# Optimization experiments

Hardware: AMD Instinct MI355X
Metric: run time of the kernel (lower is better)

## Reference

```python
import jax, jax.numpy as jnp
import numpy as np

V, E, S, TT, H, C, B = 50000, 300, 128, 12, 512, 3, 128


def setup_inputs() -> dict:
    key = jax.random.key(0)
    ks = jax.random.split(key, 12)
    sc = lambda n: 1.0 / np.sqrt(n)
    return {
        "target_ids": jax.random.randint(ks[0], (B, TT), 0, V),
        "target_len": jax.random.randint(ks[1], (B,), 1, TT + 1, dtype=jnp.int32),
        "left_ids": jax.random.randint(ks[2], (B, S), 0, V),
        "left_len": jax.random.randint(ks[3], (B,), 1, S + 1, dtype=jnp.int32),
        "right_ids": jax.random.randint(ks[4], (B, S), 0, V),
        "right_len": jax.random.randint(ks[5], (B,), 1, S + 1, dtype=jnp.int32),
        "embeddings": jax.random.normal(ks[6], (V, E), jnp.float32) * 0.1,
        "W_left": jax.random.normal(ks[7], (2 * E + H, 4 * H), jnp.float32) * sc(2 * E + H),
        "b_left": jnp.zeros((4 * H,), jnp.float32),
        "W_right": jax.random.normal(ks[8], (2 * E + H, 4 * H), jnp.float32) * sc(2 * E + H),
        "b_right": jnp.zeros((4 * H,), jnp.float32),
        "W_dense": jax.random.normal(ks[9], (2 * H, C), jnp.float32) * sc(2 * H),
        "b_dense": jnp.zeros((C,), jnp.float32),
    }


def _lstm_last_state(x, lens, W, b):
    # x: [B,S,D] inputs, lens: [B]; TF BasicLSTMCell gate order (i, j, f, o), forget_bias=1.0.
    # dynamic_rnn(sequence_length=lens): state frozen once t >= len.
    b_, s_, _ = x.shape
    xs = jnp.swapaxes(x, 0, 1)  # [S,B,D]
    step_mask = jnp.arange(s_)[:, None] < lens[None, :]  # [S,B]
    h0 = jnp.zeros((b_, H), x.dtype)
    c0 = jnp.zeros((b_, H), x.dtype)

    def step(carry, inp):
        h, c = carry
        x_t, m_t = inp
        z = jnp.concatenate([x_t, h], axis=-1) @ W + b  # [B,4H]
        i, j, f, o = jnp.split(z, 4, axis=-1)
        c_new = jax.nn.sigmoid(f + 1.0) * c + jax.nn.sigmoid(i) * jnp.tanh(j)
        h_new = jax.nn.sigmoid(o) * jnp.tanh(c_new)
        m = m_t[:, None]
        return (jnp.where(m, h_new, h), jnp.where(m, c_new, c)), None

    (h, _c), _ = jax.lax.scan(step, (h0, c0), (xs, step_mask))
    return h


def reference(target_ids, target_len, left_ids, left_len, right_ids, right_len,
              embeddings, W_left, b_left, W_right, b_right, W_dense, b_dense):
    # mean target embedding over valid target tokens (variable_len_batch_mean)
    tgt = embeddings[target_ids]  # [B,TT,E]
    tmask = (jnp.arange(TT)[None, :] < target_len[:, None]).astype(tgt.dtype)
    mean_t = jnp.sum(tgt * tmask[:, :, None], axis=1) / target_len[:, None].astype(tgt.dtype)  # [B,E]

    def ctx_inputs(ids):
        e = embeddings[ids]  # [B,S,E]
        # stack([emb, mean_t], axis=2) then reshape -> per-timestep concat [emb_t, mean_t]
        return jnp.concatenate([e, jnp.broadcast_to(mean_t[:, None, :], e.shape)], axis=-1)  # [B,S,2E]

    h_l = _lstm_last_state(ctx_inputs(left_ids), left_len, W_left, b_left)
    h_r = _lstm_last_state(ctx_inputs(right_ids), right_len, W_right, b_right)
    logits = jnp.concatenate([h_l, h_r], axis=-1) @ W_dense + b_dense  # [B,C]
    return logits
```

## Files before the change

kernel.cpp:

```cpp
#include <hip/hip_runtime.h>

#define NB 128
#define NS 128
#define NT 12
#define NE 300
#define NH 512
#define NCOL 2048
#define WGSC __HIP_MEMORY_SCOPE_WORKGROUP

typedef _Float16 h8v __attribute__((ext_vector_type(8)));
typedef __attribute__((ext_vector_type(4))) float f4v;
typedef __attribute__((ext_vector_type(4))) int   i4v;

__device__ __forceinline__ unsigned short f2h(float f) {
  union { _Float16 h; unsigned short u; } c; c.h = (_Float16)f; return c.u;
}
__device__ __forceinline__ float sigm(float x) { return 1.f / (1.f + __expf(-x)); }
__device__ __forceinline__ float tanh_(float x) { const float e = __expf(2.f * x); return 1.f - 2.f / (e + 1.f); }

__device__ __forceinline__ unsigned packh(float a, float b, int tag) {
  unsigned lo = f2h(a), hi = f2h(b);
  lo = (lo & ~1u) | (unsigned)(tag & 1);
  hi = (hi & ~1u) | (unsigned)((tag >> 1) & 1);
  return lo | (hi << 16);
}

__device__ __forceinline__ void st32f_uc(float* p, float v) {
  asm volatile("global_store_dword %0, %1, off sc1" :: "v"(p), "v"(v) : "memory");
}
__device__ __forceinline__ void st32i_uc(int* p, int v) {
  asm volatile("global_store_dword %0, %1, off sc1" :: "v"(p), "v"(v) : "memory");
}
__device__ __forceinline__ void st32u_uc(unsigned* p, unsigned v) {
  asm volatile("global_store_dword %0, %1, off sc1" :: "v"(p), "v"(v) : "memory");
}
__device__ __forceinline__ int ldflag(const int* p) {
  int v;
  asm volatile("global_load_dword %0, %1, off sc1\n\ts_waitcnt vmcnt(0)" : "=v"(v) : "v"(p) : "memory");
  return v;
}
__device__ __forceinline__ void ld64_uc(const char* a, i4v* r) {
  asm volatile(
    "global_load_dwordx4 %0, %4, off sc1\n\t"
    "global_load_dwordx4 %1, %4, off offset:16 sc1\n\t"
    "global_load_dwordx4 %2, %4, off offset:32 sc1\n\t"
    "global_load_dwordx4 %3, %4, off offset:48 sc1\n\t"
    "s_waitcnt vmcnt(0)"
    : "=&v"(r[0]), "=&v"(r[1]), "=&v"(r[2]), "=&v"(r[3])
    : "v"(a) : "memory");
}

struct Params {
  const int *tids, *tlen, *lids, *llen, *rids, *rlen;
  const float *emb, *Wl, *bl, *Wr, *br, *Wd, *bd;
  float* out;
  unsigned short* hbuf;
  float* hfin;
  int* bar;
};

__device__ __forceinline__ void lspin(int* c, int tgt) {
  while (__hip_atomic_load(c, __ATOMIC_RELAXED, WGSC) < tgt) {}
  __builtin_amdgcn_fence(__ATOMIC_ACQUIRE, "workgroup");
}
__device__ __forceinline__ void larrive(int* c) {
  __hip_atomic_fetch_add(c, 1, __ATOMIC_ACQ_REL, WGSC);
}

#define OFF_HS   0
#define OFF_XS   16384
#define OFF_ZX   26624
#define OFF_ZS   51200
#define OFF_WTH  51200
#define OFF_WTX  34816
#define LDS_SZ   59392

__global__ __launch_bounds__(512, 1) void lstm_all(Params p) {
  __shared__ __align__(16) char lds[LDS_SZ];
  __shared__ int lenL[16];
  __shared__ float redL[8][4];
  __shared__ int cnt[8];

  const int tid = threadIdx.x;
  const int wid = blockIdx.x;
  if (tid < 8) cnt[tid] = 0;

  const int g = wid & 15, ht = wid >> 4;
  const int side = g & 1, bt = g >> 1;
  const int b0 = bt * 16, d0c = ht * 32;
  const int* lenp = side ? p.rlen : p.llen;
  const int* gids = side ? p.rids : p.lids;
  const float* W = side ? p.Wr : p.Wl;
  const float* bias = side ? p.br : p.bl;
  int* fl = p.bar + g * 1024;

  const bool isH = tid < 256;
  const int wv = tid >> 6;
  const int ln = tid & 63;
  const int lwv = isH ? wv : (wv - 4);
  const int kgrp = ln >> 4;
  const int stid = tid & 255;

  float* meanTT = (float*)lds;
  float* zS = (float*)(lds + OFF_ZS);

  {
    const int r = tid >> 5, l32 = tid & 31;
    const int b = b0 + r;
    const int Lt = p.tlen[b];
    const float inv = 1.f / (float)Lt;
    int toks[NT];
    #pragma unroll
    for (int t = 0; t < NT; ++t) toks[t] = p.tids[b * NT + t];
    for (int k = l32; k < NE; k += 32) {
      float s = 0.f;
      #pragma unroll
      for (int t = 0; t < NT; ++t)
        if (t < Lt) s += p.emb[(size_t)toks[t] * NE + k];
      meanTT[k * 16 + r] = s * inv;
    }
    if (tid < 16) lenL[tid] = lenp[b0 + tid];
  }
  __syncthreads();

  if (isH) {
    const int row_c = stid >> 4;
    const int m = stid & 15;

    float zb1[4], zb2[4];
    {
      #pragma unroll
      for (int gq = 0; gq < 4; ++gq) {
        const float* wp = W + (size_t)NE * NCOL + gq * NH + d0c;
        float a1 = bias[gq * NH + d0c + 2 * m];
        float a2 = bias[gq * NH + d0c + 2 * m + 1];
        for (int k = 0; k < NE; ++k) {
          const float mv = meanTT[k * 16 + row_c];
          a1 += mv * wp[(size_t)k * NCOL + 2 * m];
          a2 += mv * wp[(size_t)k * NCOL + 2 * m + 1];
        }
        zb1[gq] = a1; zb2[gq] = a2;
      }
    }
    if (ln == 0) larrive(&cnt[6]);

    int he = 0;
    auto hpbar = [&]() {
      ++he;
      if (ln == 0) larrive(&cnt[7]);
      while (__hip_atomic_load(&cnt[7], __ATOMIC_RELAXED, WGSC) < 4 * he) {}
      __builtin_amdgcn_fence(__ATOMIC_ACQUIRE, "workgroup");
    };
    h8v hfr0[16], hfr1[16];
    {
      unsigned short* wT = (unsigned short*)(lds + OFF_WTH);
      const int r3 = stid >> 3;
      const int part = stid & 7;
      const int gate_p = part >> 1, half_p = part & 1;
      for (int i = 0; i < 16; ++i) {
        const int k = 600 + i * 32 + r3;
        const float* wr = W + (size_t)k * NCOL + gate_p * NH + d0c + half_p * 16;
        const f4v a0 = *(const f4v*)wr;
        const f4v a1 = *(const f4v*)(wr + 4);
        const f4v a2 = *(const f4v*)(wr + 8);
        const f4v a3 = *(const f4v*)(wr + 12);
        #pragma unroll
        for (int j = 0; j < 4; ++j) {
          wT[(part * 16 + j) * 32 + r3]      = f2h(a0[j]);
          wT[(part * 16 + 4 + j) * 32 + r3]  = f2h(a1[j]);
          wT[(part * 16 + 8 + j) * 32 + r3]  = f2h(a2[j]);
          wT[(part * 16 + 12 + j) * 32 + r3] = f2h(a3[j]);
        }
        hpbar();
        const int c0 = lwv * 32 + (ln & 15);
        hfr0[i] = *(const h8v*)((char*)wT + c0 * 64 + kgrp * 16);
        hfr1[i] = *(const h8v*)((char*)wT + (c0 + 16) * 64 + kgrp * 16);
        hpbar();
      }
    }

    float cR1 = 0.f, cR2 = 0.f, hR1 = 0.f, hR2 = 0.f;
    const int a_r = ln & 15;
    const int srow = stid >> 4;
    const int schk = stid & 15;
    for (int t = 0; t < NS; ++t) {
      lspin(&cnt[2], 4 * (t + 1));
      const float* zx = (const float*)(lds + OFF_ZX + (t % 3) * 8192);
      f4v acc0, acc1;
      #pragma unroll
      for (int rg = 0; rg < 4; ++rg) {
        const int rr = kgrp * 4 + rg;
        acc0[rg] = zx[rr * 128 + lwv * 32 + (ln & 15)];
        acc1[rg] = zx[rr * 128 + lwv * 32 + 16 + (ln & 15)];
      }
      if (ln == 0) larrive(&cnt[3]);

      if (t) {
        const char* src = (const char*)(p.hbuf
            + (size_t)(((t & 1) * 2 + side) * NB + b0 + srow) * NH + schk * 32);
        const unsigned exp32 = ((unsigned)(t & 1)) | (((unsigned)((t >> 1) & 1)) << 16);
        i4v v[4];
        for (;;) {
          ld64_uc(src, v);
          unsigned bad = 0;
          #pragma unroll
          for (int q = 0; q < 4; ++q)
            #pragma unroll
            for (int j = 0; j < 4; ++j)
              bad |= (((unsigned)v[q][j]) ^ exp32) & 0x00010001u;
          if (!bad) break;
        }
        #pragma unroll
        for (int q = 0; q < 4; ++q) {
          const int c16 = schk * 4 + q;
          *(i4v*)(lds + OFF_HS + srow * 1024 + ((c16 * 16) ^ ((srow & 7) << 4))) = v[q];
        }
        if (ln == 0) larrive(&cnt[0]);
        while (__hip_atomic_load(&cnt[0], __ATOMIC_RELAXED, WGSC) < 4 * t) {}
        __builtin_amdgcn_fence(__ATOMIC_ACQUIRE, "workgroup");
        #pragma unroll
        for (int kt = 0; kt < 16; ++kt) {
          h8v a = *(const h8v*)(lds + OFF_HS + a_r * 1024
                                + (((kt * 4 + kgrp) * 16) ^ ((a_r & 7) << 4)));
          acc0 = __builtin_amdgcn_mfma_f32_16x16x32_f16(a, hfr0[kt], acc0, 0, 0, 0);
          acc1 = __builtin_amdgcn_mfma_f32_16x16x32_f16(a, hfr1[kt], acc1, 0, 0, 0);
        }
      }

      #pragma unroll
      for (int rg = 0; rg < 4; ++rg) {
        const int rr = kgrp * 4 + rg;
        zS[rr * 128 + lwv * 32 + (ln & 15)]      = acc0[rg];
        zS[rr * 128 + lwv * 32 + 16 + (ln & 15)] = acc1[rg];
      }
      if (ln == 0) larrive(&cnt[4]);
      while (__hip_atomic_load(&cnt[4], __ATOMIC_RELAXED, WGSC) < 4 * (t + 1)) {}
      __builtin_amdgcn_fence(__ATOMIC_ACQUIRE, "workgroup");

      {
        const float* zr = zS + row_c * 128;
        float zi = zr[0 * 32 + 2 * m] + zb1[0], zj = zr[1 * 32 + 2 * m] + zb1[1];
        float zf = zr[2 * 32 + 2 * m] + zb1[2], zo = zr[3 * 32 + 2 * m] + zb1[3];
        float ig = sigm(zi), jg = tanh_(zj), fg = sigm(zf + 1.f), og = sigm(zo);
        float cn = fg * cR1 + ig * jg;
        float hn = og * tanh_(cn);
        if (t < lenL[row_c]) { cR1 = cn; hR1 = hn; }
        zi = zr[0 * 32 + 2 * m + 1] + zb2[0]; zj = zr[1 * 32 + 2 * m + 1] + zb2[1];
        zf = zr[2 * 32 + 2 * m + 1] + zb2[2]; zo = zr[3 * 32 + 2 * m + 1] + zb2[3];
        ig = sigm(zi); jg = tanh_(zj); fg = sigm(zf + 1.f); og = sigm(zo);
        cn = fg * cR2 + ig * jg; hn = og * tanh_(cn);
        if (t < lenL[row_c]) { cR2 = cn; hR2 = hn; }
        unsigned pk = packh(hR1, hR2, (t + 1) & 3);
        unsigned* dst = (unsigned*)p.hbuf
            + ((size_t)((((t + 1) & 1) * 2 + side) * NB + b0 + row_c) * (NH / 2)) + d0c / 2 + m;
        st32u_uc(dst, pk);
      }
    }

    st32f_uc(&p.hfin[((size_t)side * NB + b0 + row_c) * NH + d0c + 2 * m], hR1);
    st32f_uc(&p.hfin[((size_t)side * NB + b0 + row_c) * NH + d0c + 2 * m + 1], hR2);
    asm volatile("s_waitcnt vmcnt(0)" ::: "memory");
    if (ln == 0) larrive(&cnt[5]);
    if (lwv == 0) {
      while (__hip_atomic_load(&cnt[5], __ATOMIC_RELAXED, WGSC) < 4) {}
      if (ln == 0) st32i_uc(fl + ht, NS + 1);
    }
  } else {
    int xe = 0;
    auto xbar = [&]() {
      ++xe;
      if (ln == 0) larrive(&cnt[1]);
      while (__hip_atomic_load(&cnt[1], __ATOMIC_RELAXED, WGSC) < 4 * xe) {}
      __builtin_amdgcn_fence(__ATOMIC_ACQUIRE, "workgroup");
    };

    h8v xfr0[10], xfr1[10];
    {
      unsigned short* wT = (unsigned short*)(lds + OFF_WTX);
      const int r3 = stid >> 3, part = stid & 7;
      const int gate_p = part >> 1, half_p = part & 1;
      for (int i = 0; i < 10; ++i) {
        const int k = i * 32 + r3;
        float v[16];
        if (k < NE) {
          const float* wr = W + (size_t)k * NCOL + gate_p * NH + d0c + half_p * 16;
          const f4v a0 = *(const f4v*)wr;
          const f4v a1 = *(const f4v*)(wr + 4);
          const f4v a2 = *(const f4v*)(wr + 8);
          const f4v a3 = *(const f4v*)(wr + 12);
          #pragma unroll
          for (int j = 0; j < 4; ++j) {
            v[j] = a0[j]; v[4 + j] = a1[j]; v[8 + j] = a2[j]; v[12 + j] = a3[j];
          }
        } else {
          #pragma unroll
          for (int j = 0; j < 16; ++j) v[j] = 0.f;
        }
        #pragma unroll
        for (int j = 0; j < 16; ++j)
          wT[(part * 16 + j) * 32 + r3] = f2h(v[j]);
        xbar();
        const int c0 = lwv * 32 + (ln & 15);
        xfr0[i] = *(const h8v*)((char*)wT + c0 * 64 + kgrp * 16);
        xfr1[i] = *(const h8v*)((char*)wT + (c0 + 16) * 64 + kgrp * 16);
        xbar();
      }
    }

    lspin(&cnt[6], 4);

    for (int n = 0; n < NS; ++n) {
      if (n >= 3) lspin(&cnt[3], 4 * (n - 2));
      {
        const int xrow = stid >> 4;
        const int tok = gids[(size_t)(b0 + xrow) * NS + n];
        const float* ep_ = p.emb + (size_t)tok * NE;
        #pragma unroll
        for (int j = 0; j < 3; ++j) {
          const int c16 = (stid & 15) + j * 16;
          if (c16 < 40) {
            unsigned short tmp[8];
            if (c16 < 37) {
              const f4v v0 = *(const f4v*)(ep_ + c16 * 8);
              const f4v v1 = *(const f4v*)(ep_ + c16 * 8 + 4);
              tmp[0] = f2h(v0[0]); tmp[1] = f2h(v0[1]); tmp[2] = f2h(v0[2]); tmp[3] = f2h(v0[3]);
              tmp[4] = f2h(v1[0]); tmp[5] = f2h(v1[1]); tmp[6] = f2h(v1[2]); tmp[7] = f2h(v1[3]);
            } else if (c16 == 37) {
              const f4v v0 = *(const f4v*)(ep_ + 296);
              tmp[0] = f2h(v0[0]); tmp[1] = f2h(v0[1]); tmp[2] = f2h(v0[2]); tmp[3] = f2h(v0[3]);
              tmp[4] = 0; tmp[5] = 0; tmp[6] = 0; tmp[7] = 0;
            } else {
              #pragma unroll
              for (int q = 0; q < 8; ++q) tmp[q] = 0;
            }
            *(i4v*)(lds + OFF_XS + xrow * 640 + ((c16 * 16) ^ ((xrow & 7) << 4))) = *(const i4v*)tmp;
          }
        }
      }
      xbar();
      f4v a0 = {0.f, 0.f, 0.f, 0.f}, a1 = {0.f, 0.f, 0.f, 0.f};
      const int a_r = ln & 15;
      #pragma unroll
      for (int kt = 0; kt < 10; ++kt) {
        h8v a = *(const h8v*)(lds + OFF_XS + a_r * 640
                              + (((kt * 4 + kgrp) * 16) ^ ((a_r & 7) << 4)));
        a0 = __builtin_amdgcn_mfma_f32_16x16x32_f16(a, xfr0[kt], a0, 0, 0, 0);
        a1 = __builtin_amdgcn_mfma_f32_16x16x32_f16(a, xfr1[kt], a1, 0, 0, 0);
      }
      float* zx = (float*)(lds + OFF_ZX + (n % 3) * 8192);
      #pragma unroll
      for (int rg = 0; rg < 4; ++rg) {
        const int rr = kgrp * 4 + rg;
        zx[rr * 128 + lwv * 32 + (ln & 15)]      = a0[rg];
        zx[rr * 128 + lwv * 32 + 16 + (ln & 15)] = a1[rg];
      }
      if (ln == 0) larrive(&cnt[2]);
      xbar();
    }
  }

  if (wid < NB) {
    const int b = wid, bth = b >> 4;
    if (tid < 32) {
      const int gh = (bth << 1) + (tid >> 4);
      const int* f = p.bar + gh * 1024 + (tid & 15);
      int v = ldflag(f);
      while (__ballot(v < NS + 1) != 0ull) { __builtin_amdgcn_s_sleep(2); v = ldflag(f); }
    }
    __syncthreads();

    float a0 = 0.f, a1 = 0.f, a2 = 0.f;
    #pragma unroll
    for (int q = 0; q < 2; ++q) {
      const int kk = q * 512 + tid;
      const int hs = kk >> 9, dim = kk & 511;
      const float* hp = &p.hfin[((size_t)hs * NB + b) * NH + dim];
      const float hv = __hip_atomic_load(hp, __ATOMIC_RELAXED, __HIP_MEMORY_SCOPE_AGENT);
      a0 += hv * p.Wd[kk * 3 + 0];
      a1 += hv * p.Wd[kk * 3 + 1];
      a2 += hv * p.Wd[kk * 3 + 2];
    }
    #pragma unroll
    for (int s = 32; s > 0; s >>= 1) {
      a0 += __shfl_down(a0, s, 64);
      a1 += __shfl_down(a1, s, 64);
      a2 += __shfl_down(a2, s, 64);
    }
    if (ln == 0) { redL[wv][0] = a0; redL[wv][1] = a1; redL[wv][2] = a2; }
    __syncthreads();
    if (tid == 0) {
      float o0 = p.bd[0], o1 = p.bd[1], o2 = p.bd[2];
      #pragma unroll
      for (int w = 0; w < 8; ++w) { o0 += redL[w][0]; o1 += redL[w][1]; o2 += redL[w][2]; }
      p.out[b * 3 + 0] = o0;
      p.out[b * 3 + 1] = o1;
      p.out[b * 3 + 2] = o2;
    }
  }
}

extern "C" void kernel_launch(void* const* d_in, const int* in_sizes, int n_in,
                              void* d_out, int out_size, void* d_ws, size_t ws_size,
                              hipStream_t stream) {
  (void)in_sizes; (void)n_in; (void)out_size; (void)ws_size;
  char* ws = (char*)d_ws;
  Params p;
  p.tids = (const int*)d_in[0];
  p.tlen = (const int*)d_in[1];
  p.lids = (const int*)d_in[2];
  p.llen = (const int*)d_in[3];
  p.rids = (const int*)d_in[4];
  p.rlen = (const int*)d_in[5];
  p.emb  = (const float*)d_in[6];
  p.Wl   = (const float*)d_in[7];
  p.bl   = (const float*)d_in[8];
  p.Wr   = (const float*)d_in[9];
  p.br   = (const float*)d_in[10];
  p.Wd   = (const float*)d_in[11];
  p.bd   = (const float*)d_in[12];
  p.out  = (float*)d_out;
  p.bar  = (int*)ws;
  p.hbuf = (unsigned short*)(ws + 65536);
  p.hfin = (float*)(ws + 65536 + 524288);
  hipMemsetAsync(ws, 0, 65536 + 524288, stream);
  lstm_all<<<dim3(256), dim3(512), 0, stream>>>(p);
}
```

Baseline: 435.1 us.

## Load recurrent h fragments directly into registers and keep gate math wave-local

The h-side waves now load their MFMA A-operand fragments for the previous hidden state straight from global memory into registers, sized to match the fragment layout. This drops the staging copy through LDS and the workgroup barrier that came after it. The weight columns and the zx layout are permuted so each wave owns complete i/j/f/o gate groups for its own 8 hidden dims. Gate nonlinearities then read from a per-wave LDS scratch with only an lgkmcnt wait instead of a cross-wave barrier. The cost is more VGPRs (16 x i4v per lane) and redundant global loads, since each wave now re-reads all of h rather than a quarter of it.

```diff
diff --git a/kernel.cpp b/kernel.cpp
--- a/kernel.cpp
+++ b/kernel.cpp
@@ -39,14 +39,29 @@
   asm volatile("global_load_dword %0, %1, off sc1\n\ts_waitcnt vmcnt(0)" : "=v"(v) : "v"(p) : "memory");
   return v;
 }
-__device__ __forceinline__ void ld64_uc(const char* a, i4v* r) {
+__device__ __forceinline__ void ld16_uc(const char* a, i4v* r) {
   asm volatile(
-    "global_load_dwordx4 %0, %4, off sc1\n\t"
-    "global_load_dwordx4 %1, %4, off offset:16 sc1\n\t"
-    "global_load_dwordx4 %2, %4, off offset:32 sc1\n\t"
-    "global_load_dwordx4 %3, %4, off offset:48 sc1\n\t"
+    "global_load_dwordx4 %0, %16, off sc1\n\t"
+    "global_load_dwordx4 %1, %16, off offset:64 sc1\n\t"
+    "global_load_dwordx4 %2, %16, off offset:128 sc1\n\t"
+    "global_load_dwordx4 %3, %16, off offset:192 sc1\n\t"
+    "global_load_dwordx4 %4, %16, off offset:256 sc1\n\t"
+    "global_load_dwordx4 %5, %16, off offset:320 sc1\n\t"
+    "global_load_dwordx4 %6, %16, off offset:384 sc1\n\t"
+    "global_load_dwordx4 %7, %16, off offset:448 sc1\n\t"
+    "global_load_dwordx4 %8, %16, off offset:512 sc1\n\t"
+    "global_load_dwordx4 %9, %16, off offset:576 sc1\n\t"
+    "global_load_dwordx4 %10, %16, off offset:640 sc1\n\t"
+    "global_load_dwordx4 %11, %16, off offset:704 sc1\n\t"
+    "global_load_dwordx4 %12, %16, off offset:768 sc1\n\t"
+    "global_load_dwordx4 %13, %16, off offset:832 sc1\n\t"
+    "global_load_dwordx4 %14, %16, off offset:896 sc1\n\t"
+    "global_load_dwordx4 %15, %16, off offset:960 sc1\n\t"
     "s_waitcnt vmcnt(0)"
-    : "=&v"(r[0]), "=&v"(r[1]), "=&v"(r[2]), "=&v"(r[3])
+    : "=&v"(r[0]), "=&v"(r[1]), "=&v"(r[2]), "=&v"(r[3]),
+      "=&v"(r[4]), "=&v"(r[5]), "=&v"(r[6]), "=&v"(r[7]),
+      "=&v"(r[8]), "=&v"(r[9]), "=&v"(r[10]), "=&v"(r[11]),
+      "=&v"(r[12]), "=&v"(r[13]), "=&v"(r[14]), "=&v"(r[15])
     : "v"(a) : "memory");
 }
 
@@ -67,13 +82,12 @@
   __hip_atomic_fetch_add(c, 1, __ATOMIC_ACQ_REL, WGSC);
 }
 
-#define OFF_HS   0
-#define OFF_XS   16384
-#define OFF_ZX   26624
-#define OFF_ZS   51200
-#define OFF_WTH  51200
-#define OFF_WTX  34816
-#define LDS_SZ   59392
+#define OFF_XS   0
+#define OFF_ZX   10240
+#define OFF_ZW   34816
+#define OFF_WTH  34816
+#define OFF_WTX  26624
+#define LDS_SZ   44032
 
 __global__ __launch_bounds__(512, 1) void lstm_all(Params p) {
   __shared__ __align__(16) char lds[LDS_SZ];
@@ -102,7 +116,6 @@
   const int stid = tid & 255;
 
   float* meanTT = (float*)lds;
-  float* zS = (float*)(lds + OFF_ZS);
 
   {
     const int r = tid >> 5, l32 = tid & 31;
@@ -124,22 +137,24 @@
   __syncthreads();
 
   if (isH) {
-    const int row_c = stid >> 4;
-    const int m = stid & 15;
-
-    float zb1[4], zb2[4];
+    const int c = ln & 15;
+    const int crow = ln >> 2;
+    const int dj0 = (ln & 3) * 2;
+    const int gdim = d0c + lwv * 8 + dj0;
+
+    float zb[8];
     {
       #pragma unroll
       for (int gq = 0; gq < 4; ++gq) {
-        const float* wp = W + (size_t)NE * NCOL + gq * NH + d0c;
-        float a1 = bias[gq * NH + d0c + 2 * m];
-        float a2 = bias[gq * NH + d0c + 2 * m + 1];
+        const float* wp = W + (size_t)NE * NCOL + gq * NH + gdim;
+        float a1 = bias[gq * NH + gdim];
+        float a2 = bias[gq * NH + gdim + 1];
         for (int k = 0; k < NE; ++k) {
-          const float mv = meanTT[k * 16 + row_c];
-          a1 += mv * wp[(size_t)k * NCOL + 2 * m];
-          a2 += mv * wp[(size_t)k * NCOL + 2 * m + 1];
-        }
-        zb1[gq] = a1; zb2[gq] = a2;
+          const float mv = meanTT[k * 16 + crow];
+          a1 += mv * wp[(size_t)k * NCOL];
+          a2 += mv * wp[(size_t)k * NCOL + 1];
+        }
+        zb[gq * 2] = a1; zb[gq * 2 + 1] = a2;
       }
     }
     if (ln == 0) larrive(&cnt[6]);
@@ -157,6 +172,8 @@
       const int r3 = stid >> 3;
       const int part = stid & 7;
       const int gate_p = part >> 1, half_p = part & 1;
+      const int L0 = (c >> 3) * 32 + lwv * 8 + (c & 7);
+      const int L1 = L0 + 64;
       for (int i = 0; i < 16; ++i) {
         const int k = 600 + i * 32 + r3;
         const float* wr = W + (size_t)k * NCOL + gate_p * NH + d0c + half_p * 16;
@@ -172,17 +189,16 @@
           wT[(part * 16 + 12 + j) * 32 + r3] = f2h(a3[j]);
         }
         hpbar();
-        const int c0 = lwv * 32 + (ln & 15);
-        hfr0[i] = *(const h8v*)((char*)wT + c0 * 64 + kgrp * 16);
-        hfr1[i] = *(const h8v*)((char*)wT + (c0 + 16) * 64 + kgrp * 16);
+        hfr0[i] = *(const h8v*)((char*)wT + L0 * 64 + kgrp * 16);
+        hfr1[i] = *(const h8v*)((char*)wT + L1 * 64 + kgrp * 16);
         hpbar();
       }
     }
 
     float cR1 = 0.f, cR2 = 0.f, hR1 = 0.f, hR2 = 0.f;
-    const int a_r = ln & 15;
-    const int srow = stid >> 4;
-    const int schk = stid & 15;
+    float* zW = (float*)(lds + OFF_ZW + lwv * 2304);
+    const int zc = (lwv * 8 + (c & 7)) * 4;
+    const int ga = c >> 3;
     for (int t = 0; t < NS; ++t) {
       lspin(&cnt[2], 4 * (t + 1));
       const float* zx = (const float*)(lds + OFF_ZX + (t % 3) * 8192);
@@ -190,38 +206,29 @@
       #pragma unroll
       for (int rg = 0; rg < 4; ++rg) {
         const int rr = kgrp * 4 + rg;
-        acc0[rg] = zx[rr * 128 + lwv * 32 + (ln & 15)];
-        acc1[rg] = zx[rr * 128 + lwv * 32 + 16 + (ln & 15)];
+        acc0[rg] = zx[rr * 128 + zc + ga];
+        acc1[rg] = zx[rr * 128 + zc + 2 + ga];
       }
       if (ln == 0) larrive(&cnt[3]);
 
       if (t) {
         const char* src = (const char*)(p.hbuf
-            + (size_t)(((t & 1) * 2 + side) * NB + b0 + srow) * NH + schk * 32);
+            + (size_t)(((t & 1) * 2 + side) * NB + b0 + c) * NH) + kgrp * 16;
         const unsigned exp32 = ((unsigned)(t & 1)) | (((unsigned)((t >> 1) & 1)) << 16);
-        i4v v[4];
+        i4v v[16];
         for (;;) {
-          ld64_uc(src, v);
+          ld16_uc(src, v);
           unsigned bad = 0;
           #pragma unroll
-          for (int q = 0; q < 4; ++q)
+          for (int q = 0; q < 16; ++q)
             #pragma unroll
             for (int j = 0; j < 4; ++j)
               bad |= (((unsigned)v[q][j]) ^ exp32) & 0x00010001u;
-          if (!bad) break;
-        }
-        #pragma unroll
-        for (int q = 0; q < 4; ++q) {
-          const int c16 = schk * 4 + q;
-          *(i4v*)(lds + OFF_HS + srow * 1024 + ((c16 * 16) ^ ((srow & 7) << 4))) = v[q];
-        }
-        if (ln == 0) larrive(&cnt[0]);
-        while (__hip_atomic_load(&cnt[0], __ATOMIC_RELAXED, WGSC) < 4 * t) {}
-        __builtin_amdgcn_fence(__ATOMIC_ACQUIRE, "workgroup");
+          if (__ballot(bad != 0) == 0ull) break;
+        }
         #pragma unroll
         for (int kt = 0; kt < 16; ++kt) {
-          h8v a = *(const h8v*)(lds + OFF_HS + a_r * 1024
-                                + (((kt * 4 + kgrp) * 16) ^ ((a_r & 7) << 4)));
+          h8v a = __builtin_bit_cast(h8v, v[kt]);
           acc0 = __builtin_amdgcn_mfma_f32_16x16x32_f16(a, hfr0[kt], acc0, 0, 0, 0);
           acc1 = __builtin_amdgcn_mfma_f32_16x16x32_f16(a, hfr1[kt], acc1, 0, 0, 0);
         }
@@ -230,35 +237,34 @@
       #pragma unroll
       for (int rg = 0; rg < 4; ++rg) {
         const int rr = kgrp * 4 + rg;
-        zS[rr * 128 + lwv * 32 + (ln & 15)]      = acc0[rg];
-        zS[rr * 128 + lwv * 32 + 16 + (ln & 15)] = acc1[rg];
-      }
-      if (ln == 0) larrive(&cnt[4]);
-      while (__hip_atomic_load(&cnt[4], __ATOMIC_RELAXED, WGSC) < 4 * (t + 1)) {}
-      __builtin_amdgcn_fence(__ATOMIC_ACQUIRE, "workgroup");
+        zW[rr * 36 + c]      = acc0[rg];
+        zW[rr * 36 + 16 + c] = acc1[rg];
+      }
+      asm volatile("s_waitcnt lgkmcnt(0)" ::: "memory");
 
       {
-        const float* zr = zS + row_c * 128;
-        float zi = zr[0 * 32 + 2 * m] + zb1[0], zj = zr[1 * 32 + 2 * m] + zb1[1];
-        float zf = zr[2 * 32 + 2 * m] + zb1[2], zo = zr[3 * 32 + 2 * m] + zb1[3];
-        float ig = sigm(zi), jg = tanh_(zj), fg = sigm(zf + 1.f), og = sigm(zo);
+        const float* zr = zW + crow * 36;
+        float zi1 = zr[dj0]      + zb[0], zi2 = zr[dj0 + 1]      + zb[1];
+        float zj1 = zr[8 + dj0]  + zb[2], zj2 = zr[8 + dj0 + 1]  + zb[3];
+        float zf1 = zr[16 + dj0] + zb[4], zf2 = zr[16 + dj0 + 1] + zb[5];
+        float zo1 = zr[24 + dj0] + zb[6], zo2 = zr[24 + dj0 + 1] + zb[7];
+        float ig = sigm(zi1), jg = tanh_(zj1), fg = sigm(zf1 + 1.f), og = sigm(zo1);
         float cn = fg * cR1 + ig * jg;
         float hn = og * tanh_(cn);
-        if (t < lenL[row_c]) { cR1 = cn; hR1 = hn; }
-        zi = zr[0 * 32 + 2 * m + 1] + zb2[0]; zj = zr[1 * 32 + 2 * m + 1] + zb2[1];
-        zf = zr[2 * 32 + 2 * m + 1] + zb2[2]; zo = zr[3 * 32 + 2 * m + 1] + zb2[3];
-        ig = sigm(zi); jg = tanh_(zj); fg = sigm(zf + 1.f); og = sigm(zo);
+        if (t < lenL[crow]) { cR1 = cn; hR1 = hn; }
+        ig = sigm(zi2); jg = tanh_(zj2); fg = sigm(zf2 + 1.f); og = sigm(zo2);
         cn = fg * cR2 + ig * jg; hn = og * tanh_(cn);
-        if (t < lenL[row_c]) { cR2 = cn; hR2 = hn; }
+        if (t < lenL[crow]) { cR2 = cn; hR2 = hn; }
         unsigned pk = packh(hR1, hR2, (t + 1) & 3);
         unsigned* dst = (unsigned*)p.hbuf
-            + ((size_t)((((t + 1) & 1) * 2 + side) * NB + b0 + row_c) * (NH / 2)) + d0c / 2 + m;
+            + ((size_t)((((t + 1) & 1) * 2 + side) * NB + b0 + crow) * (NH / 2))
+            + gdim / 2;
         st32u_uc(dst, pk);
       }
     }
 
-    st32f_uc(&p.hfin[((size_t)side * NB + b0 + row_c) * NH + d0c + 2 * m], hR1);
-    st32f_uc(&p.hfin[((size_t)side * NB + b0 + row_c) * NH + d0c + 2 * m + 1], hR2);
+    st32f_uc(&p.hfin[((size_t)side * NB + b0 + crow) * NH + gdim], hR1);
+    st32f_uc(&p.hfin[((size_t)side * NB + b0 + crow) * NH + gdim + 1], hR2);
     asm volatile("s_waitcnt vmcnt(0)" ::: "memory");
     if (ln == 0) larrive(&cnt[5]);
     if (lwv == 0) {
@@ -351,8 +357,8 @@
       #pragma unroll
       for (int rg = 0; rg < 4; ++rg) {
         const int rr = kgrp * 4 + rg;
-        zx[rr * 128 + lwv * 32 + (ln & 15)]      = a0[rg];
-        zx[rr * 128 + lwv * 32 + 16 + (ln & 15)] = a1[rg];
+        zx[rr * 128 + (ln & 15) * 4 + lwv]        = a0[rg];
+        zx[rr * 128 + (16 + (ln & 15)) * 4 + lwv] = a1[rg];
       }
       if (ln == 0) larrive(&cnt[2]);
       xbar();
```

Result: slower. 591.0 us (+35.8%).
